# Optimization experiments

Measured on AMD Instinct MI355X. Metric: run time of the kernel, lower is better.

Reference implementation:

```python
import jax, jax.numpy as jnp
import numpy as np

B, S, D, H = 4, 2048, 1024, 16
DK = D // H
NEG = -1e9


def setup_inputs() -> dict:
    key = jax.random.key(0)
    ks = jax.random.split(key, 8)
    q = jax.random.normal(ks[0], (B, S, D), dtype=jnp.float32)
    k = jax.random.normal(ks[1], (B, S, D), dtype=jnp.float32)
    v = jax.random.normal(ks[2], (B, S, D), dtype=jnp.float32)
    # causal mask, broadcastable to [B,H,S,S]; mask==0 -> masked out
    mask = jnp.tril(jnp.ones((S, S), dtype=jnp.int32))[None, None, :, :]
    scale = 1.0 / np.sqrt(D)
    w_q = jax.random.normal(ks[3], (D, D), dtype=jnp.float32) * scale
    w_k = jax.random.normal(ks[4], (D, D), dtype=jnp.float32) * scale
    w_v = jax.random.normal(ks[5], (D, D), dtype=jnp.float32) * scale
    w_o = jax.random.normal(ks[6], (D, D), dtype=jnp.float32) * scale
    return {"q": q, "k": k, "v": v, "mask": mask,
            "w_q": w_q, "w_k": w_k, "w_v": w_v, "w_o": w_o}


def reference(q, k, v, mask, w_q, w_k, w_v, w_o):
    # projections (nn.Linear with no bias: x @ W^T)
    def proj(x, w):
        y = jnp.einsum('bsd,ed->bse', x, w)          # [B,S,D]
        return y.reshape(B, -1, H, DK).transpose(0, 2, 1, 3)  # [B,H,S,DK]
    Q, K, V = proj(q, w_q), proj(k, w_k), proj(v, w_v)
    scores = jnp.einsum('bhqd,bhkd->bhqk', Q, K) * (DK ** -0.5)  # [B,H,S,S]
    scores = jnp.where(mask == 0, NEG, scores)
    attn = jax.nn.softmax(scores, axis=-1)
    x = jnp.einsum('bhqk,bhkd->bhqd', attn, V)       # [B,H,S,DK]
    x = x.transpose(0, 2, 1, 3).reshape(B, -1, D)    # [B,S,D]
    return jnp.einsum('bsd,ed->bse', x, w_o)
```

## Files before the change

### kernel.cpp

```cpp
#include <hip/hip_runtime.h>
#include <hip/hip_bf16.h>
#include <stdint.h>

#define B_ 4
#define S_ 2048
#define D_ 1024
#define H_ 16
#define DK_ 64

typedef __hip_bfloat16 bf16;
typedef __attribute__((ext_vector_type(8))) __bf16 bf16x8;
typedef __attribute__((ext_vector_type(4))) __bf16 bf16x4;
typedef __attribute__((ext_vector_type(4))) float f32x4;
typedef __attribute__((ext_vector_type(4))) uint32_t u32x4;

#define QSCALE 0.18033688011112042f

__device__ __forceinline__ void async_copy16(const void* g, void* l) {
    __builtin_amdgcn_global_load_lds((const __attribute__((address_space(1))) void*)g,
                                     (__attribute__((address_space(3))) void*)l,
                                     16, 0, 0);
}

__device__ __forceinline__ bf16x8 ld8(const bf16* p) {
    return *(const bf16x8*)p;
}

__device__ __forceinline__ uint32_t pk2(float a, float b) {
    union { __bf16 h; uint16_t u; } x, y;
    x.h = (__bf16)a; y.h = (__bf16)b;
    return (uint32_t)x.u | ((uint32_t)y.u << 16);
}

__device__ __forceinline__ bf16x8 cvt8(float4 u0, float4 u1) {
    return (bf16x8){(__bf16)u0.x, (__bf16)u0.y, (__bf16)u0.z, (__bf16)u0.w,
                    (__bf16)u1.x, (__bf16)u1.y, (__bf16)u1.z, (__bf16)u1.w};
}

__device__ __forceinline__ bf16x8 transpose_p(const float* p0, const float* p1,
                                              int srcl, bool loT) {
    uint32_t x0 = pk2(p0[0], p0[1]), x1 = pk2(p0[2], p0[3]);
    uint32_t y0 = pk2(p1[0], p1[1]), y1 = pk2(p1[2], p1[3]);
    u32x4 dw;
#pragma unroll
    for (int i = 0; i < 4; i++) {
        int sl = srcl + (i >> 1) * 16;
        uint32_t vA = (uint32_t)__shfl((int)((i & 1) ? x1 : x0), sl, 64);
        uint32_t vB = (uint32_t)__shfl((int)((i & 1) ? y1 : y0), sl, 64);
        dw[i] = loT ? vA : vB;
    }
    return __builtin_bit_cast(bf16x8, dw);
}

__global__ __launch_bounds__(256) void cvtw(const float4* __restrict__ s0,
                                            const float4* __restrict__ s1,
                                            const float4* __restrict__ s2,
                                            const float4* __restrict__ s3,
                                            bf16x4* __restrict__ d0,
                                            bf16x4* __restrict__ d1,
                                            bf16x4* __restrict__ d2,
                                            bf16x4* __restrict__ d3) {
    int i = blockIdx.x * 256 + threadIdx.x;
    int seg = i >> 18;
    int j   = i & 262143;
    const float4* s = seg == 0 ? s0 : seg == 1 ? s1 : seg == 2 ? s2 : s3;
    bf16x4*       d = seg == 0 ? d0 : seg == 1 ? d1 : seg == 2 ? d2 : d3;
    float4 f = s[j];
    d[j] = (bf16x4){(__bf16)f.x, (__bf16)f.y, (__bf16)f.z, (__bf16)f.w};
}

__global__ __launch_bounds__(256) void cvtx(const float* __restrict__ s0,
                                            const float* __restrict__ s1,
                                            const float* __restrict__ s2,
                                            bf16* __restrict__ d0,
                                            bf16* __restrict__ d1,
                                            bf16* __restrict__ d2) {
    const int z = blockIdx.z;
    const float* s = z == 0 ? s0 : z == 1 ? s1 : s2;
    bf16*        d = z == 0 ? d0 : z == 1 ? d1 : d2;
    size_t i = ((size_t)blockIdx.x * 256 + threadIdx.x) * 8;
    float4 u0 = *(const float4*)(s + i);
    float4 u1 = *(const float4*)(s + i + 4);
    *(bf16x8*)(d + i) = cvt8(u0, u1);
}

__global__ __launch_bounds__(256) void gemm_qkv_bf(const bf16* __restrict__ Aq,
                                                   const bf16* __restrict__ Ak,
                                                   const bf16* __restrict__ Av,
                                                   const bf16* __restrict__ Wqb,
                                                   const bf16* __restrict__ Wkb,
                                                   const bf16* __restrict__ Wvb,
                                                   bf16* __restrict__ Oq,
                                                   bf16* __restrict__ Ok,
                                                   bf16* __restrict__ Ov) {
    __shared__ bf16 lA[128 * 32];
    __shared__ bf16 lW[128 * 32];
    const int z = blockIdx.z;
    const bf16* A = z == 0 ? Aq : z == 1 ? Ak : Av;
    const bf16* W = z == 0 ? Wqb : z == 1 ? Wkb : Wvb;
    bf16*      out = z == 0 ? Oq : z == 1 ? Ok : Ov;

    const int tid  = threadIdx.x;
    const int lane = tid & 63;
    const int quad = lane >> 4;
    const int lo   = lane & 15;
    const int wave = tid >> 6;
    const int wm   = (wave >> 1) * 64;
    const int wn   = (wave & 1) * 64;
    const int n0   = blockIdx.x * 128;
    const int m0   = blockIdx.y * 128;
    const int K    = 1024;

    f32x4 acc[4][4];
#pragma unroll
    for (int i = 0; i < 4; i++)
#pragma unroll
        for (int j = 0; j < 4; j++) acc[i][j] = (f32x4){0.f, 0.f, 0.f, 0.f};

    const int sr = tid >> 2;
    const int sc = (tid & 3) * 8;

    for (int k0 = 0; k0 < K; k0 += 32) {
        async_copy16(A + (size_t)(m0 + sr) * K + k0 + sc,       lA + sr * 32 + sc);
        async_copy16(A + (size_t)(m0 + 64 + sr) * K + k0 + sc,  lA + (64 + sr) * 32 + sc);
        async_copy16(W + (size_t)(n0 + sr) * K + k0 + sc,       lW + sr * 32 + sc);
        async_copy16(W + (size_t)(n0 + 64 + sr) * K + k0 + sc,  lW + (64 + sr) * 32 + sc);
        __syncthreads();

        bf16x8 af[4], bfr[4];
#pragma unroll
        for (int i = 0; i < 4; i++)
            af[i] = ld8(lA + (wm + i * 16 + lo) * 32 + quad * 8);
#pragma unroll
        for (int j = 0; j < 4; j++)
            bfr[j] = ld8(lW + (wn + j * 16 + lo) * 32 + quad * 8);
#pragma unroll
        for (int i = 0; i < 4; i++)
#pragma unroll
            for (int j = 0; j < 4; j++)
                acc[i][j] = __builtin_amdgcn_mfma_f32_16x16x32_bf16(af[i], bfr[j], acc[i][j], 0, 0, 0);
        __syncthreads();
    }

#pragma unroll
    for (int i = 0; i < 4; i++)
#pragma unroll
        for (int j = 0; j < 4; j++)
#pragma unroll
            for (int r = 0; r < 4; r++) {
                int m = m0 + wm + i * 16 + quad * 4 + r;
                int n = n0 + wn + j * 16 + lo;
                float val = acc[i][j][r];
                int b = m >> 11, s = m & (S_ - 1);
                int h = n >> 6, dk = n & 63;
                if (z == 0) {
                    out[((size_t)(b * H_ + h) * S_ + s) * DK_ + dk] =
                        __float2bfloat16(val * QSCALE);
                } else if (z == 1) {
                    out[((size_t)(b * H_ + h) * S_ + s) * DK_ + dk] = __float2bfloat16(val);
                } else {
                    out[((size_t)(b * H_ + h) * DK_ + dk) * S_ + s] = __float2bfloat16(val);
                }
            }
}

__global__ __launch_bounds__(256) void gemm_qkv(const float* __restrict__ Aq,
                                                const float* __restrict__ Ak,
                                                const float* __restrict__ Av,
                                                const bf16* __restrict__ Wqb,
                                                const bf16* __restrict__ Wkb,
                                                const bf16* __restrict__ Wvb,
                                                bf16* __restrict__ Oq,
                                                bf16* __restrict__ Ok,
                                                bf16* __restrict__ Ov) {
    __shared__ bf16 lA[128 * 32];
    __shared__ bf16 lW[128 * 32];
    const int z = blockIdx.z;
    const float* A = z == 0 ? Aq : z == 1 ? Ak : Av;
    const bf16*  W = z == 0 ? Wqb : z == 1 ? Wkb : Wvb;
    bf16*      out = z == 0 ? Oq : z == 1 ? Ok : Ov;

    const int tid  = threadIdx.x;
    const int lane = tid & 63;
    const int quad = lane >> 4;
    const int lo   = lane & 15;
    const int wave = tid >> 6;
    const int wm   = (wave >> 1) * 64;
    const int wn   = (wave & 1) * 64;
    const int n0   = blockIdx.x * 128;
    const int m0   = blockIdx.y * 128;
    const int K    = 1024;

    f32x4 acc[4][4];
#pragma unroll
    for (int i = 0; i < 4; i++)
#pragma unroll
        for (int j = 0; j < 4; j++) acc[i][j] = (f32x4){0.f, 0.f, 0.f, 0.f};

    const int sr = tid >> 2;
    const int sc = (tid & 3) * 8;

    for (int k0 = 0; k0 < K; k0 += 32) {
        async_copy16(W + (size_t)(n0 + sr) * K + k0 + sc,       lW + sr * 32 + sc);
        async_copy16(W + (size_t)(n0 + 64 + sr) * K + k0 + sc,  lW + (64 + sr) * 32 + sc);
        const float* a0 = A + (size_t)(m0 + sr) * K + k0 + sc;
        const float* a1 = A + (size_t)(m0 + 64 + sr) * K + k0 + sc;
        float4 u0 = *(const float4*)a0;
        float4 u1 = *(const float4*)(a0 + 4);
        float4 u2 = *(const float4*)a1;
        float4 u3 = *(const float4*)(a1 + 4);
        *(bf16x8*)(lA + sr * 32 + sc)        = cvt8(u0, u1);
        *(bf16x8*)(lA + (64 + sr) * 32 + sc) = cvt8(u2, u3);
        __syncthreads();

        bf16x8 af[4], bfr[4];
#pragma unroll
        for (int i = 0; i < 4; i++)
            af[i] = ld8(lA + (wm + i * 16 + lo) * 32 + quad * 8);
#pragma unroll
        for (int j = 0; j < 4; j++)
            bfr[j] = ld8(lW + (wn + j * 16 + lo) * 32 + quad * 8);
#pragma unroll
        for (int i = 0; i < 4; i++)
#pragma unroll
            for (int j = 0; j < 4; j++)
                acc[i][j] = __builtin_amdgcn_mfma_f32_16x16x32_bf16(af[i], bfr[j], acc[i][j], 0, 0, 0);
        __syncthreads();
    }

#pragma unroll
    for (int i = 0; i < 4; i++)
#pragma unroll
        for (int j = 0; j < 4; j++)
#pragma unroll
            for (int r = 0; r < 4; r++) {
                int m = m0 + wm + i * 16 + quad * 4 + r;
                int n = n0 + wn + j * 16 + lo;
                float val = acc[i][j][r];
                int b = m >> 11, s = m & (S_ - 1);
                int h = n >> 6, dk = n & 63;
                if (z == 0) {
                    out[((size_t)(b * H_ + h) * S_ + s) * DK_ + dk] =
                        __float2bfloat16(val * QSCALE);
                } else if (z == 1) {
                    out[((size_t)(b * H_ + h) * S_ + s) * DK_ + dk] = __float2bfloat16(val);
                } else {
                    out[((size_t)(b * H_ + h) * DK_ + dk) * S_ + s] = __float2bfloat16(val);
                }
            }
}

__global__ __launch_bounds__(256) void gemm_out(const bf16* __restrict__ A,
                                                const bf16* __restrict__ W,
                                                float* __restrict__ out) {
    __shared__ bf16 lA[128 * 32];
    __shared__ bf16 lW[128 * 32];
    const int tid  = threadIdx.x;
    const int lane = tid & 63;
    const int quad = lane >> 4;
    const int lo   = lane & 15;
    const int wave = tid >> 6;
    const int wm   = (wave >> 1) * 64;
    const int wn   = (wave & 1) * 64;
    const int n0   = blockIdx.x * 128;
    const int m0   = blockIdx.y * 128;
    const int K    = 1024;

    f32x4 acc[4][4];
#pragma unroll
    for (int i = 0; i < 4; i++)
#pragma unroll
        for (int j = 0; j < 4; j++) acc[i][j] = (f32x4){0.f, 0.f, 0.f, 0.f};

    const int sr = tid >> 2;
    const int sc = (tid & 3) * 8;

    for (int k0 = 0; k0 < K; k0 += 32) {
        async_copy16(A + (size_t)(m0 + sr) * K + k0 + sc,       lA + sr * 32 + sc);
        async_copy16(A + (size_t)(m0 + 64 + sr) * K + k0 + sc,  lA + (64 + sr) * 32 + sc);
        async_copy16(W + (size_t)(n0 + sr) * K + k0 + sc,       lW + sr * 32 + sc);
        async_copy16(W + (size_t)(n0 + 64 + sr) * K + k0 + sc,  lW + (64 + sr) * 32 + sc);
        __syncthreads();

        bf16x8 af[4], bfr[4];
#pragma unroll
        for (int i = 0; i < 4; i++)
            af[i] = ld8(lA + (wm + i * 16 + lo) * 32 + quad * 8);
#pragma unroll
        for (int j = 0; j < 4; j++)
            bfr[j] = ld8(lW + (wn + j * 16 + lo) * 32 + quad * 8);
#pragma unroll
        for (int i = 0; i < 4; i++)
#pragma unroll
            for (int j = 0; j < 4; j++)
                acc[i][j] = __builtin_amdgcn_mfma_f32_16x16x32_bf16(af[i], bfr[j], acc[i][j], 0, 0, 0);
        __syncthreads();
    }

#pragma unroll
    for (int i = 0; i < 4; i++)
#pragma unroll
        for (int j = 0; j < 4; j++)
#pragma unroll
            for (int r = 0; r < 4; r++) {
                int m = m0 + wm + i * 16 + quad * 4 + r;
                int n = n0 + wn + j * 16 + lo;
                out[(size_t)m * D_ + n] = acc[i][j][r];
            }
}

__global__ __launch_bounds__(64) void attn(const bf16* __restrict__ Q,
                                           const bf16* __restrict__ K,
                                           const bf16* __restrict__ Vt,
                                           bf16* __restrict__ X) {
    const int lane = threadIdx.x;
    const int quad = lane >> 4;
    const int lo   = lane & 15;
    const int idx  = blockIdx.x;
    const int bh   = idx & 63;
    const int qb   = 63 - (idx >> 6);
    const int q0   = qb * 32;

    const bf16* Qp = Q  + (size_t)bh * S_ * DK_;
    const bf16* Kp = K  + (size_t)bh * S_ * DK_;
    const bf16* Vp = Vt + (size_t)bh * DK_ * S_;

    bf16x8 bQa0 = ld8(Qp + (size_t)(q0 + lo) * DK_ + quad * 8);
    bf16x8 bQa1 = ld8(Qp + (size_t)(q0 + lo) * DK_ + 32 + quad * 8);
    bf16x8 bQb0 = ld8(Qp + (size_t)(q0 + 16 + lo) * DK_ + quad * 8);
    bf16x8 bQb1 = ld8(Qp + (size_t)(q0 + 16 + lo) * DK_ + 32 + quad * 8);

    f32x4 outA[4], outB[4];
#pragma unroll
    for (int t = 0; t < 4; t++) {
        outA[t] = (f32x4){0.f, 0.f, 0.f, 0.f};
        outB[t] = (f32x4){0.f, 0.f, 0.f, 0.f};
    }
    float lsumA = 0.f, lsumB = 0.f;

    const int nfull = qb;
    const int srcl  = (quad & 1) * 32 + lo;
    const bool loT  = (quad < 2);

    const bf16* kp0 = Kp + (size_t)lo * DK_ + quad * 8;
    bf16x8 a00 = ld8(kp0), a01 = ld8(kp0 + 32);
    bf16x8 a10 = ld8(kp0 + 16 * DK_), a11 = ld8(kp0 + 16 * DK_ + 32);

    for (int it = 0; it <= nfull; ++it) {
        const int kv0 = it * 32;
        const bool masked = (it == nfull);

        bf16x8 aV[4];
#pragma unroll
        for (int t = 0; t < 4; t++)
            aV[t] = ld8(Vp + (size_t)(t * 16 + lo) * S_ + kv0 + quad * 8);

        f32x4 stA0 = (f32x4){0.f,0.f,0.f,0.f}, stA1 = (f32x4){0.f,0.f,0.f,0.f};
        f32x4 stB0 = (f32x4){0.f,0.f,0.f,0.f}, stB1 = (f32x4){0.f,0.f,0.f,0.f};
        stA0 = __builtin_amdgcn_mfma_f32_16x16x32_bf16(a00, bQa0, stA0, 0, 0, 0);
        stA0 = __builtin_amdgcn_mfma_f32_16x16x32_bf16(a01, bQa1, stA0, 0, 0, 0);
        stA1 = __builtin_amdgcn_mfma_f32_16x16x32_bf16(a10, bQa0, stA1, 0, 0, 0);
        stA1 = __builtin_amdgcn_mfma_f32_16x16x32_bf16(a11, bQa1, stA1, 0, 0, 0);
        stB0 = __builtin_amdgcn_mfma_f32_16x16x32_bf16(a00, bQb0, stB0, 0, 0, 0);
        stB0 = __builtin_amdgcn_mfma_f32_16x16x32_bf16(a01, bQb1, stB0, 0, 0, 0);
        stB1 = __builtin_amdgcn_mfma_f32_16x16x32_bf16(a10, bQb0, stB1, 0, 0, 0);
        stB1 = __builtin_amdgcn_mfma_f32_16x16x32_bf16(a11, bQb1, stB1, 0, 0, 0);

        {
            const int kvn = masked ? kv0 : kv0 + 32;
            const bf16* kn = Kp + (size_t)(kvn + lo) * DK_ + quad * 8;
            a00 = ld8(kn); a01 = ld8(kn + 32);
            a10 = ld8(kn + 16 * DK_); a11 = ld8(kn + 16 * DK_ + 32);
        }

        float pA0[4], pA1[4], pB0[4], pB1[4];
#pragma unroll
        for (int r = 0; r < 4; r++) {
            float eA0 = exp2f(stA0[r]);
            float eA1 = exp2f(stA1[r]);
            float eB0 = exp2f(stB0[r]);
            float eB1 = exp2f(stB1[r]);
            if (masked) {
                bool c = (quad * 4 + r) <= lo;
                eA0 = c ? eA0 : 0.f;
                eA1 = 0.f;
                eB1 = c ? eB1 : 0.f;
            }
            pA0[r] = eA0; pA1[r] = eA1; pB0[r] = eB0; pB1[r] = eB1;
            lsumA += eA0 + eA1;
            lsumB += eB0 + eB1;
        }

        bf16x8 bPA = transpose_p(pA0, pA1, srcl, loT);
        bf16x8 bPB = transpose_p(pB0, pB1, srcl, loT);

#pragma unroll
        for (int t = 0; t < 4; t++) {
            outA[t] = __builtin_amdgcn_mfma_f32_16x16x32_bf16(aV[t], bPA, outA[t], 0, 0, 0);
            outB[t] = __builtin_amdgcn_mfma_f32_16x16x32_bf16(aV[t], bPB, outB[t], 0, 0, 0);
        }
    }

    lsumA += __shfl_xor(lsumA, 16, 64);
    lsumA += __shfl_xor(lsumA, 32, 64);
    lsumB += __shfl_xor(lsumB, 16, 64);
    lsumB += __shfl_xor(lsumB, 32, 64);
    const float rlA = 1.f / lsumA;
    const float rlB = 1.f / lsumB;

    const int b = bh >> 4, h = bh & 15;
    bf16* XpA = X + (size_t)(b * S_ + q0 + lo) * D_ + h * 64;
    bf16* XpB = XpA + (size_t)16 * D_;
#pragma unroll
    for (int t = 0; t < 4; t++) {
        uint32_t* dA = (uint32_t*)(XpA + t * 16 + quad * 4);
        dA[0] = pk2(outA[t][0] * rlA, outA[t][1] * rlA);
        dA[1] = pk2(outA[t][2] * rlA, outA[t][3] * rlA);
        uint32_t* dB = (uint32_t*)(XpB + t * 16 + quad * 4);
        dB[0] = pk2(outB[t][0] * rlB, outB[t][1] * rlB);
        dB[1] = pk2(outB[t][2] * rlB, outB[t][3] * rlB);
    }
}

extern "C" void kernel_launch(void* const* d_in, const int* in_sizes, int n_in,
                              void* d_out, int out_size, void* d_ws, size_t ws_size,
                              hipStream_t stream) {
    const float* q  = (const float*)d_in[0];
    const float* k  = (const float*)d_in[1];
    const float* v  = (const float*)d_in[2];
    const float* wq = (const float*)d_in[4];
    const float* wk = (const float*)d_in[5];
    const float* wv = (const float*)d_in[6];
    const float* wo = (const float*)d_in[7];

    const size_t elems  = (size_t)B_ * S_ * D_;
    const size_t welems = (size_t)D_ * D_;
    bf16* WoB = (bf16*)d_ws;
    bf16* WqB = WoB + welems;
    bf16* WkB = WqB + welems;
    bf16* WvB = WkB + welems;
    bf16* Xb  = WqB;
    bf16* Qw  = WqB + elems;
    bf16* Kw  = Qw + elems;
    bf16* Vw  = Kw + elems;
    bf16* Aqb = Vw + elems;
    bf16* Akb = Aqb + elems;
    bf16* Avb = Akb + elems;

    const size_t need_big = ((size_t)(Avb + elems) - (size_t)d_ws);

    hipLaunchKernelGGL(cvtw, dim3(4 * (int)(welems / 4) / 256), dim3(256), 0, stream,
                       (const float4*)wq, (const float4*)wk, (const float4*)wv,
                       (const float4*)wo,
                       (bf16x4*)WqB, (bf16x4*)WkB, (bf16x4*)WvB, (bf16x4*)WoB);

    if (ws_size >= need_big) {
        hipLaunchKernelGGL(cvtx, dim3((int)(elems / 8 / 256), 1, 3), dim3(256), 0, stream,
                           q, k, v, Aqb, Akb, Avb);
        hipLaunchKernelGGL(gemm_qkv_bf, dim3(D_ / 128, (B_ * S_) / 128, 3), dim3(256), 0,
                           stream, Aqb, Akb, Avb, WqB, WkB, WvB, Qw, Kw, Vw);
    } else {
        hipLaunchKernelGGL(gemm_qkv, dim3(D_ / 128, (B_ * S_) / 128, 3), dim3(256), 0,
                           stream, q, k, v, WqB, WkB, WvB, Qw, Kw, Vw);
    }

    hipLaunchKernelGGL(attn, dim3((S_ / 32) * B_ * H_), dim3(64), 0, stream, Qw, Kw, Vw, Xb);
    hipLaunchKernelGGL(gemm_out, dim3(D_ / 128, (B_ * S_) / 128), dim3(256), 0, stream,
                       Xb, WoB, (float*)d_out);
}
```

Baseline: 410.8 us.

## Software-pipeline QK^T one tile ahead in attention kernel with ping-pong K registers

Restructures the attention inner loop into a two-stage software pipeline. The QK^T MFMAs for the next KV tile are issued before the softmax and PV work of the current tile, with even/odd K register sets and a two-tile-ahead K prefetch. This is meant to hide MFMA latency and the dependency between score computation and exp/transpose. It also swaps exp2f for the raw hardware exp2 builtin and adds a min-waves launch bound, which raises register pressure and risks spills.

Measured after the change: 446.8 us. 8.8% more time.

```diff
diff --git a/kernel.cpp b/kernel.cpp
--- a/kernel.cpp
+++ b/kernel.cpp
@@ -15,6 +15,15 @@
 typedef __attribute__((ext_vector_type(4))) uint32_t u32x4;
 
 #define QSCALE 0.18033688011112042f
+
+#if defined(__has_builtin)
+#if __has_builtin(__builtin_amdgcn_exp2f)
+#define EXP2(x) __builtin_amdgcn_exp2f(x)
+#endif
+#endif
+#ifndef EXP2
+#define EXP2(x) exp2f(x)
+#endif
 
 __device__ __forceinline__ void async_copy16(const void* g, void* l) {
     __builtin_amdgcn_global_load_lds((const __attribute__((address_space(1))) void*)g,
@@ -309,10 +318,81 @@
             }
 }
 
-__global__ __launch_bounds__(64) void attn(const bf16* __restrict__ Q,
-                                           const bf16* __restrict__ K,
-                                           const bf16* __restrict__ Vt,
-                                           bf16* __restrict__ X) {
+
+__device__ __forceinline__ void loadK4(const bf16* __restrict__ Kp, int kv, int lo, int quad,
+                                       bf16x8& k0, bf16x8& k1, bf16x8& k2, bf16x8& k3) {
+    const bf16* kn = Kp + (size_t)(kv + lo) * DK_ + quad * 8;
+    k0 = ld8(kn);
+    k1 = ld8(kn + 32);
+    k2 = ld8(kn + 16 * DK_);
+    k3 = ld8(kn + 16 * DK_ + 32);
+}
+
+__device__ __forceinline__ void qk8(const bf16x8& k0, const bf16x8& k1,
+                                    const bf16x8& k2, const bf16x8& k3,
+                                    const bf16x8& bQa0, const bf16x8& bQa1,
+                                    const bf16x8& bQb0, const bf16x8& bQb1,
+                                    f32x4& s0, f32x4& s1, f32x4& s2, f32x4& s3) {
+    s0 = (f32x4){0.f, 0.f, 0.f, 0.f};
+    s1 = (f32x4){0.f, 0.f, 0.f, 0.f};
+    s2 = (f32x4){0.f, 0.f, 0.f, 0.f};
+    s3 = (f32x4){0.f, 0.f, 0.f, 0.f};
+    s0 = __builtin_amdgcn_mfma_f32_16x16x32_bf16(k0, bQa0, s0, 0, 0, 0);
+    s0 = __builtin_amdgcn_mfma_f32_16x16x32_bf16(k1, bQa1, s0, 0, 0, 0);
+    s1 = __builtin_amdgcn_mfma_f32_16x16x32_bf16(k2, bQa0, s1, 0, 0, 0);
+    s1 = __builtin_amdgcn_mfma_f32_16x16x32_bf16(k3, bQa1, s1, 0, 0, 0);
+    s2 = __builtin_amdgcn_mfma_f32_16x16x32_bf16(k0, bQb0, s2, 0, 0, 0);
+    s2 = __builtin_amdgcn_mfma_f32_16x16x32_bf16(k1, bQb1, s2, 0, 0, 0);
+    s3 = __builtin_amdgcn_mfma_f32_16x16x32_bf16(k2, bQb0, s3, 0, 0, 0);
+    s3 = __builtin_amdgcn_mfma_f32_16x16x32_bf16(k3, bQb1, s3, 0, 0, 0);
+}
+
+__device__ __forceinline__ void sfpv(int it, int nfull, const bf16* __restrict__ Vp,
+                                     int lo, int quad, int srcl, bool loT,
+                                     const f32x4& s0, const f32x4& s1,
+                                     const f32x4& s2, const f32x4& s3,
+                                     f32x4 (&outA)[4], f32x4 (&outB)[4],
+                                     float& lsumA, float& lsumB) {
+    const int kv0 = it * 32;
+    const bool masked = (it == nfull);
+
+    bf16x8 aV[4];
+#pragma unroll
+    for (int t = 0; t < 4; t++)
+        aV[t] = ld8(Vp + (size_t)(t * 16 + lo) * S_ + kv0 + quad * 8);
+
+    float pA0[4], pA1[4], pB0[4], pB1[4];
+#pragma unroll
+    for (int r = 0; r < 4; r++) {
+        float eA0 = EXP2(s0[r]);
+        float eA1 = EXP2(s1[r]);
+        float eB0 = EXP2(s2[r]);
+        float eB1 = EXP2(s3[r]);
+        if (masked) {
+            bool c = (quad * 4 + r) <= lo;
+            eA0 = c ? eA0 : 0.f;
+            eA1 = 0.f;
+            eB1 = c ? eB1 : 0.f;
+        }
+        pA0[r] = eA0; pA1[r] = eA1; pB0[r] = eB0; pB1[r] = eB1;
+        lsumA += eA0 + eA1;
+        lsumB += eB0 + eB1;
+    }
+
+    bf16x8 bPA = transpose_p(pA0, pA1, srcl, loT);
+    bf16x8 bPB = transpose_p(pB0, pB1, srcl, loT);
+
+#pragma unroll
+    for (int t = 0; t < 4; t++) {
+        outA[t] = __builtin_amdgcn_mfma_f32_16x16x32_bf16(aV[t], bPA, outA[t], 0, 0, 0);
+        outB[t] = __builtin_amdgcn_mfma_f32_16x16x32_bf16(aV[t], bPB, outB[t], 0, 0, 0);
+    }
+}
+
+__global__ __launch_bounds__(64, 4) void attn(const bf16* __restrict__ Q,
+                                              const bf16* __restrict__ K,
+                                              const bf16* __restrict__ Vt,
+                                              bf16* __restrict__ X) {
     const int lane = threadIdx.x;
     const int quad = lane >> 4;
     const int lo   = lane & 15;
@@ -339,66 +419,34 @@
     float lsumA = 0.f, lsumB = 0.f;
 
     const int nfull = qb;
+    const int NT    = nfull + 1;
     const int srcl  = (quad & 1) * 32 + lo;
     const bool loT  = (quad < 2);
 
-    const bf16* kp0 = Kp + (size_t)lo * DK_ + quad * 8;
-    bf16x8 a00 = ld8(kp0), a01 = ld8(kp0 + 32);
-    bf16x8 a10 = ld8(kp0 + 16 * DK_), a11 = ld8(kp0 + 16 * DK_ + 32);
-
-    for (int it = 0; it <= nfull; ++it) {
-        const int kv0 = it * 32;
-        const bool masked = (it == nfull);
-
-        bf16x8 aV[4];
-#pragma unroll
-        for (int t = 0; t < 4; t++)
-            aV[t] = ld8(Vp + (size_t)(t * 16 + lo) * S_ + kv0 + quad * 8);
-
-        f32x4 stA0 = (f32x4){0.f,0.f,0.f,0.f}, stA1 = (f32x4){0.f,0.f,0.f,0.f};
-        f32x4 stB0 = (f32x4){0.f,0.f,0.f,0.f}, stB1 = (f32x4){0.f,0.f,0.f,0.f};
-        stA0 = __builtin_amdgcn_mfma_f32_16x16x32_bf16(a00, bQa0, stA0, 0, 0, 0);
-        stA0 = __builtin_amdgcn_mfma_f32_16x16x32_bf16(a01, bQa1, stA0, 0, 0, 0);
-        stA1 = __builtin_amdgcn_mfma_f32_16x16x32_bf16(a10, bQa0, stA1, 0, 0, 0);
-        stA1 = __builtin_amdgcn_mfma_f32_16x16x32_bf16(a11, bQa1, stA1, 0, 0, 0);
-        stB0 = __builtin_amdgcn_mfma_f32_16x16x32_bf16(a00, bQb0, stB0, 0, 0, 0);
-        stB0 = __builtin_amdgcn_mfma_f32_16x16x32_bf16(a01, bQb1, stB0, 0, 0, 0);
-        stB1 = __builtin_amdgcn_mfma_f32_16x16x32_bf16(a10, bQb0, stB1, 0, 0, 0);
-        stB1 = __builtin_amdgcn_mfma_f32_16x16x32_bf16(a11, bQb1, stB1, 0, 0, 0);
-
+    bf16x8 kE0, kE1, kE2, kE3, kO0, kO1, kO2, kO3;
+    f32x4 sE0, sE1, sE2, sE3, sO0, sO1, sO2, sO3;
+
+    loadK4(Kp, 0, lo, quad, kE0, kE1, kE2, kE3);
+    qk8(kE0, kE1, kE2, kE3, bQa0, bQa1, bQb0, bQb1, sE0, sE1, sE2, sE3);
+    loadK4(Kp, (NT > 1 ? 32 : 0), lo, quad, kO0, kO1, kO2, kO3);
+
+    for (int it = 0; it < NT; it += 2) {
+        qk8(kO0, kO1, kO2, kO3, bQa0, bQa1, bQb0, bQb1, sO0, sO1, sO2, sO3);
         {
-            const int kvn = masked ? kv0 : kv0 + 32;
-            const bf16* kn = Kp + (size_t)(kvn + lo) * DK_ + quad * 8;
-            a00 = ld8(kn); a01 = ld8(kn + 32);
-            a10 = ld8(kn + 16 * DK_); a11 = ld8(kn + 16 * DK_ + 32);
+            int kv2 = it + 2; if (kv2 > nfull) kv2 = nfull;
+            loadK4(Kp, kv2 * 32, lo, quad, kE0, kE1, kE2, kE3);
         }
-
-        float pA0[4], pA1[4], pB0[4], pB1[4];
-#pragma unroll
-        for (int r = 0; r < 4; r++) {
-            float eA0 = exp2f(stA0[r]);
-            float eA1 = exp2f(stA1[r]);
-            float eB0 = exp2f(stB0[r]);
-            float eB1 = exp2f(stB1[r]);
-            if (masked) {
-                bool c = (quad * 4 + r) <= lo;
-                eA0 = c ? eA0 : 0.f;
-                eA1 = 0.f;
-                eB1 = c ? eB1 : 0.f;
-            }
-            pA0[r] = eA0; pA1[r] = eA1; pB0[r] = eB0; pB1[r] = eB1;
-            lsumA += eA0 + eA1;
-            lsumB += eB0 + eB1;
+        sfpv(it, nfull, Vp, lo, quad, srcl, loT, sE0, sE1, sE2, sE3,
+             outA, outB, lsumA, lsumB);
+        if (it + 1 >= NT) break;
+
+        qk8(kE0, kE1, kE2, kE3, bQa0, bQa1, bQb0, bQb1, sE0, sE1, sE2, sE3);
+        {
+            int kv3 = it + 3; if (kv3 > nfull) kv3 = nfull;
+            loadK4(Kp, kv3 * 32, lo, quad, kO0, kO1, kO2, kO3);
         }
-
-        bf16x8 bPA = transpose_p(pA0, pA1, srcl, loT);
-        bf16x8 bPB = transpose_p(pB0, pB1, srcl, loT);
-
-#pragma unroll
-        for (int t = 0; t < 4; t++) {
-            outA[t] = __builtin_amdgcn_mfma_f32_16x16x32_bf16(aV[t], bPA, outA[t], 0, 0, 0);
-            outB[t] = __builtin_amdgcn_mfma_f32_16x16x32_bf16(aV[t], bPB, outB[t], 0, 0, 0);
-        }
+        sfpv(it + 1, nfull, Vp, lo, quad, srcl, loT, sO0, sO1, sO2, sO3,
+             outA, outB, lsumA, lsumB);
     }
 
     lsumA += __shfl_xor(lsumA, 16, 64);
```

## Process 64 query rows per attention wave to reuse K/V loads

Applied to the files above, without the earlier changes.

Each single-wave attention block now handles 64 query rows (four 16-row subtiles) instead of 32, so every K and V tile loaded from global memory feeds twice as many MFMAs. The causal handling is extended with per-subtile mask modes, and the grid is halved. It also adds s_setprio around the MFMA sections and uses the raw amdgcn exp2 builtin. The cost is higher register pressure and fewer blocks, which may hurt occupancy and load balance.

New measurement: 372.8 us. 9.2% less time.

```diff
diff --git a/kernel.cpp b/kernel.cpp
--- a/kernel.cpp
+++ b/kernel.cpp
@@ -15,6 +15,15 @@
 typedef __attribute__((ext_vector_type(4))) uint32_t u32x4;
 
 #define QSCALE 0.18033688011112042f
+
+#if defined(__has_builtin)
+#if __has_builtin(__builtin_amdgcn_exp2f)
+#define EXP2(x) __builtin_amdgcn_exp2f(x)
+#endif
+#endif
+#ifndef EXP2
+#define EXP2(x) exp2f(x)
+#endif
 
 __device__ __forceinline__ void async_copy16(const void* g, void* l) {
     __builtin_amdgcn_global_load_lds((const __attribute__((address_space(1))) void*)g,
@@ -318,107 +327,121 @@
     const int lo   = lane & 15;
     const int idx  = blockIdx.x;
     const int bh   = idx & 63;
-    const int qb   = 63 - (idx >> 6);
-    const int q0   = qb * 32;
+    const int qbp  = 31 - (idx >> 6);
+    const int q0   = qbp * 64;
 
     const bf16* Qp = Q  + (size_t)bh * S_ * DK_;
     const bf16* Kp = K  + (size_t)bh * S_ * DK_;
     const bf16* Vp = Vt + (size_t)bh * DK_ * S_;
 
-    bf16x8 bQa0 = ld8(Qp + (size_t)(q0 + lo) * DK_ + quad * 8);
-    bf16x8 bQa1 = ld8(Qp + (size_t)(q0 + lo) * DK_ + 32 + quad * 8);
-    bf16x8 bQb0 = ld8(Qp + (size_t)(q0 + 16 + lo) * DK_ + quad * 8);
-    bf16x8 bQb1 = ld8(Qp + (size_t)(q0 + 16 + lo) * DK_ + 32 + quad * 8);
-
-    f32x4 outA[4], outB[4];
-#pragma unroll
-    for (int t = 0; t < 4; t++) {
-        outA[t] = (f32x4){0.f, 0.f, 0.f, 0.f};
-        outB[t] = (f32x4){0.f, 0.f, 0.f, 0.f};
-    }
-    float lsumA = 0.f, lsumB = 0.f;
-
-    const int nfull = qb;
-    const int srcl  = (quad & 1) * 32 + lo;
-    const bool loT  = (quad < 2);
-
-    const bf16* kp0 = Kp + (size_t)lo * DK_ + quad * 8;
-    bf16x8 a00 = ld8(kp0), a01 = ld8(kp0 + 32);
-    bf16x8 a10 = ld8(kp0 + 16 * DK_), a11 = ld8(kp0 + 16 * DK_ + 32);
-
-    for (int it = 0; it <= nfull; ++it) {
+    bf16x8 bQ[4][2];
+#pragma unroll
+    for (int qs = 0; qs < 4; qs++) {
+        const bf16* qp = Qp + (size_t)(q0 + qs * 16 + lo) * DK_ + quad * 8;
+        bQ[qs][0] = ld8(qp);
+        bQ[qs][1] = ld8(qp + 32);
+    }
+
+    f32x4 out[4][4];
+    float lsum[4] = {0.f, 0.f, 0.f, 0.f};
+#pragma unroll
+    for (int qs = 0; qs < 4; qs++)
+#pragma unroll
+        for (int t = 0; t < 4; t++) out[qs][t] = (f32x4){0.f, 0.f, 0.f, 0.f};
+
+    const int NT   = 2 * qbp + 2;
+    const int srcl = (quad & 1) * 32 + lo;
+    const bool loT = (quad < 2);
+
+    bf16x8 aK0, aK1, aK2, aK3;
+    {
+        const bf16* kn = Kp + (size_t)lo * DK_ + quad * 8;
+        aK0 = ld8(kn); aK1 = ld8(kn + 32);
+        aK2 = ld8(kn + 16 * DK_); aK3 = ld8(kn + 16 * DK_ + 32);
+    }
+
+    for (int it = 0; it < NT; ++it) {
         const int kv0 = it * 32;
-        const bool masked = (it == nfull);
+        const int am = (it < 2 * qbp) ? 0 : (it == 2 * qbp ? 1 : 2);
+        const int bm = (it < 2 * qbp + 1) ? 0 : 1;
 
         bf16x8 aV[4];
 #pragma unroll
         for (int t = 0; t < 4; t++)
             aV[t] = ld8(Vp + (size_t)(t * 16 + lo) * S_ + kv0 + quad * 8);
 
-        f32x4 stA0 = (f32x4){0.f,0.f,0.f,0.f}, stA1 = (f32x4){0.f,0.f,0.f,0.f};
-        f32x4 stB0 = (f32x4){0.f,0.f,0.f,0.f}, stB1 = (f32x4){0.f,0.f,0.f,0.f};
-        stA0 = __builtin_amdgcn_mfma_f32_16x16x32_bf16(a00, bQa0, stA0, 0, 0, 0);
-        stA0 = __builtin_amdgcn_mfma_f32_16x16x32_bf16(a01, bQa1, stA0, 0, 0, 0);
-        stA1 = __builtin_amdgcn_mfma_f32_16x16x32_bf16(a10, bQa0, stA1, 0, 0, 0);
-        stA1 = __builtin_amdgcn_mfma_f32_16x16x32_bf16(a11, bQa1, stA1, 0, 0, 0);
-        stB0 = __builtin_amdgcn_mfma_f32_16x16x32_bf16(a00, bQb0, stB0, 0, 0, 0);
-        stB0 = __builtin_amdgcn_mfma_f32_16x16x32_bf16(a01, bQb1, stB0, 0, 0, 0);
-        stB1 = __builtin_amdgcn_mfma_f32_16x16x32_bf16(a10, bQb0, stB1, 0, 0, 0);
-        stB1 = __builtin_amdgcn_mfma_f32_16x16x32_bf16(a11, bQb1, stB1, 0, 0, 0);
+        f32x4 st[4][2];
+        __builtin_amdgcn_s_setprio(1);
+#pragma unroll
+        for (int qs = 0; qs < 4; qs++) {
+            f32x4 t0 = (f32x4){0.f, 0.f, 0.f, 0.f};
+            f32x4 t1 = (f32x4){0.f, 0.f, 0.f, 0.f};
+            t0 = __builtin_amdgcn_mfma_f32_16x16x32_bf16(aK0, bQ[qs][0], t0, 0, 0, 0);
+            t0 = __builtin_amdgcn_mfma_f32_16x16x32_bf16(aK1, bQ[qs][1], t0, 0, 0, 0);
+            t1 = __builtin_amdgcn_mfma_f32_16x16x32_bf16(aK2, bQ[qs][0], t1, 0, 0, 0);
+            t1 = __builtin_amdgcn_mfma_f32_16x16x32_bf16(aK3, bQ[qs][1], t1, 0, 0, 0);
+            st[qs][0] = t0; st[qs][1] = t1;
+        }
+        __builtin_amdgcn_s_setprio(0);
 
         {
-            const int kvn = masked ? kv0 : kv0 + 32;
-            const bf16* kn = Kp + (size_t)(kvn + lo) * DK_ + quad * 8;
-            a00 = ld8(kn); a01 = ld8(kn + 32);
-            a10 = ld8(kn + 16 * DK_); a11 = ld8(kn + 16 * DK_ + 32);
+            int kvn = it + 1; if (kvn >= NT) kvn = NT - 1;
+            const bf16* kn = Kp + (size_t)(kvn * 32 + lo) * DK_ + quad * 8;
+            aK0 = ld8(kn); aK1 = ld8(kn + 32);
+            aK2 = ld8(kn + 16 * DK_); aK3 = ld8(kn + 16 * DK_ + 32);
         }
 
-        float pA0[4], pA1[4], pB0[4], pB1[4];
-#pragma unroll
-        for (int r = 0; r < 4; r++) {
-            float eA0 = exp2f(stA0[r]);
-            float eA1 = exp2f(stA1[r]);
-            float eB0 = exp2f(stB0[r]);
-            float eB1 = exp2f(stB1[r]);
-            if (masked) {
-                bool c = (quad * 4 + r) <= lo;
-                eA0 = c ? eA0 : 0.f;
-                eA1 = 0.f;
-                eB1 = c ? eB1 : 0.f;
+        bf16x8 bP[4];
+#pragma unroll
+        for (int pr = 0; pr < 2; pr++) {
+            const int mode = pr == 0 ? am : bm;
+            const int sl = pr * 2, sh = pr * 2 + 1;
+            float pl0[4], pl1[4], ph0[4], ph1[4];
+#pragma unroll
+            for (int r = 0; r < 4; r++) {
+                float el0 = EXP2(st[sl][0][r]);
+                float el1 = EXP2(st[sl][1][r]);
+                float eh0 = EXP2(st[sh][0][r]);
+                float eh1 = EXP2(st[sh][1][r]);
+                if (mode == 1) {
+                    bool c = (quad * 4 + r) <= lo;
+                    el0 = c ? el0 : 0.f;
+                    el1 = 0.f;
+                    eh1 = c ? eh1 : 0.f;
+                } else if (mode == 2) {
+                    el0 = 0.f; el1 = 0.f; eh0 = 0.f; eh1 = 0.f;
+                }
+                pl0[r] = el0; pl1[r] = el1; ph0[r] = eh0; ph1[r] = eh1;
+                lsum[sl] += el0 + el1;
+                lsum[sh] += eh0 + eh1;
             }
-            pA0[r] = eA0; pA1[r] = eA1; pB0[r] = eB0; pB1[r] = eB1;
-            lsumA += eA0 + eA1;
-            lsumB += eB0 + eB1;
+            bP[sl] = transpose_p(pl0, pl1, srcl, loT);
+            bP[sh] = transpose_p(ph0, ph1, srcl, loT);
         }
 
-        bf16x8 bPA = transpose_p(pA0, pA1, srcl, loT);
-        bf16x8 bPB = transpose_p(pB0, pB1, srcl, loT);
-
+        __builtin_amdgcn_s_setprio(1);
+#pragma unroll
+        for (int qs = 0; qs < 4; qs++)
+#pragma unroll
+            for (int t = 0; t < 4; t++)
+                out[qs][t] = __builtin_amdgcn_mfma_f32_16x16x32_bf16(aV[t], bP[qs], out[qs][t], 0, 0, 0);
+        __builtin_amdgcn_s_setprio(0);
+    }
+
+    const int b = bh >> 4, h = bh & 15;
+#pragma unroll
+    for (int qs = 0; qs < 4; qs++) {
+        float ls = lsum[qs];
+        ls += __shfl_xor(ls, 16, 64);
+        ls += __shfl_xor(ls, 32, 64);
+        const float rl = 1.f / ls;
+        bf16* Xp = X + (size_t)(b * S_ + q0 + qs * 16 + lo) * D_ + h * 64;
 #pragma unroll
         for (int t = 0; t < 4; t++) {
-            outA[t] = __builtin_amdgcn_mfma_f32_16x16x32_bf16(aV[t], bPA, outA[t], 0, 0, 0);
-            outB[t] = __builtin_amdgcn_mfma_f32_16x16x32_bf16(aV[t], bPB, outB[t], 0, 0, 0);
+            uint32_t* d = (uint32_t*)(Xp + t * 16 + quad * 4);
+            d[0] = pk2(out[qs][t][0] * rl, out[qs][t][1] * rl);
+            d[1] = pk2(out[qs][t][2] * rl, out[qs][t][3] * rl);
         }
-    }
-
-    lsumA += __shfl_xor(lsumA, 16, 64);
-    lsumA += __shfl_xor(lsumA, 32, 64);
-    lsumB += __shfl_xor(lsumB, 16, 64);
-    lsumB += __shfl_xor(lsumB, 32, 64);
-    const float rlA = 1.f / lsumA;
-    const float rlB = 1.f / lsumB;
-
-    const int b = bh >> 4, h = bh & 15;
-    bf16* XpA = X + (size_t)(b * S_ + q0 + lo) * D_ + h * 64;
-    bf16* XpB = XpA + (size_t)16 * D_;
-#pragma unroll
-    for (int t = 0; t < 4; t++) {
-        uint32_t* dA = (uint32_t*)(XpA + t * 16 + quad * 4);
-        dA[0] = pk2(outA[t][0] * rlA, outA[t][1] * rlA);
-        dA[1] = pk2(outA[t][2] * rlA, outA[t][3] * rlA);
-        uint32_t* dB = (uint32_t*)(XpB + t * 16 + quad * 4);
-        dB[0] = pk2(outB[t][0] * rlB, outB[t][1] * rlB);
-        dB[1] = pk2(outB[t][2] * rlB, outB[t][3] * rlB);
     }
 }
 
@@ -464,7 +487,7 @@
                            stream, q, k, v, WqB, WkB, WvB, Qw, Kw, Vw);
     }
 
-    hipLaunchKernelGGL(attn, dim3((S_ / 32) * B_ * H_), dim3(64), 0, stream, Qw, Kw, Vw, Xb);
+    hipLaunchKernelGGL(attn, dim3((S_ / 64) * B_ * H_), dim3(64), 0, stream, Qw, Kw, Vw, Xb);
     hipLaunchKernelGGL(gemm_out, dim3(D_ / 128, (B_ * S_) / 128), dim3(256), 0, stream,
                        Xb, WoB, (float*)d_out);
 }
```
